# Optimization experiments

Measured on AMD Instinct MI355X. Metric: run time of the kernel, lower is better.

Reference implementation:

```python
import jax, jax.numpy as jnp
from jax import lax
import numpy as np

KSIZE = 7
SIGMA = 5.0
ALPHA = 0.05

def _gaussian_kernel(ksize, sigma):
    ax = np.arange(ksize, dtype=np.float32) - (ksize - 1) / 2.0
    g1 = np.exp(-(ax ** 2) / (2.0 * sigma ** 2))
    k2 = np.outer(g1, g1)
    k2 = k2 / k2.sum()
    return jnp.asarray(k2, dtype=jnp.float32)

def _sobel_kernel():
    sx = np.array([[-1, 0, 1], [-2, 0, 2], [-1, 0, 1]], dtype=np.float32)
    sy = np.array([[-1, -2, -1], [0, 0, 0], [1, 2, 1]], dtype=np.float32)
    return jnp.asarray(np.stack([sx, sy])[:, None], dtype=jnp.float32)  # (2,1,3,3)

def setup_inputs() -> dict:
    key = jax.random.key(0)
    x = jax.random.normal(key, (4, 1, 2048, 2048), dtype=jnp.float32)
    return {"x": x, "sobel_k": _sobel_kernel(), "gauss_k": _gaussian_kernel(KSIZE, SIGMA)}

def reference(x, sobel_k, gauss_k):
    N, _, H, W = x.shape
    dn = ('NCHW', 'OIHW', 'NCHW')
    # Image gradients: Sobel conv, 1 -> 2 channels, same padding
    g = lax.conv_general_dilated(x, sobel_k, (1, 1), [(1, 1), (1, 1)], dimension_numbers=dn)
    Ix, Iy = g[:, 0], g[:, 1]  # (N,H,W)
    # Channel products: I_xx, I_yy, I_xy
    prods = jnp.stack([Ix * Ix, Iy * Iy, Ix * Iy], axis=1)  # (N,3,H,W)
    # Second moment: depthwise 7x7 Gaussian smoothing, same padding
    p = KSIZE // 2
    gk = jnp.broadcast_to(gauss_k[None, None], (3, 1, KSIZE, KSIZE))
    S = lax.conv_general_dilated(prods, gk, (1, 1), [(p, p), (p, p)], dimension_numbers=dn, feature_group_count=3)
    Sxx, Syy, Sxy = S[:, 0], S[:, 1], S[:, 2]
    # Corner response R = det(M) - alpha * trace(M)^2
    R = Sxx * Syy - Sxy * Sxy - ALPHA * (Sxx + Syy) ** 2  # (N,H,W)
    # NMS: global lower-median threshold (torch.median semantics), 7x7 maxpool, equality mask
    n = H * W
    med = jnp.sort(R.reshape(N, -1), axis=1)[:, (n - 1) // 2]  # torch lower median
    Rt = jnp.where(R >= med[:, None, None], R, jnp.float32(0.0))
    mx = lax.reduce_window(Rt, -jnp.inf, lax.max, (1, KSIZE, KSIZE), (1, 1, 1), [(0, 0), (p, p), (p, p)])
    out = jnp.where(Rt == mx, Rt, jnp.float32(0.0))
    return out[:, None]  # (N,1,H,W)
```

## Files before the change

### kernel.cpp

```cpp
#include <hip/hip_runtime.h>

#define H 2048
#define W 2048
#define NIMG 4
#define HWPX (H*W)
#define K_RANK 2097151u

__device__ __forceinline__ unsigned fmap(float f) {
    unsigned u = __float_as_uint(f);
    return (u & 0x80000000u) ? ~u : (u | 0x80000000u);
}

__global__ void k_prep(const float* __restrict__ gk, double* __restrict__ kwd) {
    int t = threadIdx.x;
    if (t < 49) kwd[t] = (double)gk[t];
}

__global__ __launch_bounds__(512, 4) void k_harris_R(const float* __restrict__ x,
                                                     const double* __restrict__ kwd,
                                                     float* __restrict__ R,
                                                     unsigned* __restrict__ hist1)
{
    __shared__ float xs[4096];
    __align__(16) __shared__ double ixiy[2*38*72];
    unsigned* hist = (unsigned*)xs;

    const int tid = threadIdx.x;
    const int img = blockIdx.z;
    const int x0 = blockIdx.x * 64, y0 = blockIdx.y * 32;
    const float* __restrict__ X = x + (size_t)img * HWPX;

    for (int i = tid; i < 2880; i += 512) {
        int r = i / 72, c = i - r * 72;
        int gy = y0 - 4 + r, gx = x0 - 4 + c;
        float v = 0.f;
        if ((unsigned)gy < H && (unsigned)gx < W) v = X[(size_t)gy * W + gx];
        xs[i] = v;
    }
    __syncthreads();

    for (int i = tid; i < 2736; i += 512) {
        int r = i / 72, c = i - r * 72;
        double ix = 0.0, iy = 0.0;
        int gy = y0 - 3 + r, gx = x0 - 3 + c;
        if (c < 70 && (unsigned)gy < H && (unsigned)gx < W) {
            const float* p0 = &xs[r * 72 + c];
            double x00 = p0[0],   x01 = p0[1],   x02 = p0[2];
            double x10 = p0[72],                  x12 = p0[74];
            double x20 = p0[144], x21 = p0[145], x22 = p0[146];
            ix = (x02 - x00) + 2.0 * (x12 - x10) + (x22 - x20);
            iy = (x20 - x00) + 2.0 * (x21 - x01) + (x22 - x02);
        }
        ixiy[i] = ix;
        ixiy[2736 + i] = iy;
    }
    __syncthreads();

    for (int i = tid; i < 4096; i += 512) hist[i] = 0;
    __syncthreads();

    const int tc = (tid & 31) * 2;
    const int tr = (tid >> 5) * 2;

    double axx[2][2], ayy[2][2], axy[2][2];
    #pragma unroll
    for (int rr = 0; rr < 2; rr++)
        #pragma unroll
        for (int cc = 0; cc < 2; cc++) { axx[rr][cc] = 0.0; ayy[rr][cc] = 0.0; axy[rr][cc] = 0.0; }

    #pragma unroll
    for (int ii = 0; ii < 8; ii++) {
        const int prow = tr + ii;
        double vx[8], vy[8];
        const double2* rx = (const double2*)&ixiy[prow * 72 + tc];
        const double2* ry = (const double2*)&ixiy[2736 + prow * 72 + tc];
        #pragma unroll
        for (int q = 0; q < 4; q++) {
            double2 t = rx[q]; vx[2*q] = t.x; vx[2*q+1] = t.y;
            double2 u = ry[q]; vy[2*q] = u.x; vy[2*q+1] = u.y;
        }
        double xx0 = vx[0]*vx[0], yy0 = vy[0]*vy[0], xy0 = vx[0]*vy[0];
        #pragma unroll
        for (int j = 0; j < 7; j++) {
            double xx1 = vx[j+1]*vx[j+1], yy1 = vy[j+1]*vy[j+1], xy1 = vx[j+1]*vy[j+1];
            #pragma unroll
            for (int rr = 0; rr < 2; rr++) {
                const int wrow = ii - rr;
                if (wrow >= 0 && wrow <= 6) {
                    double w = kwd[wrow * 7 + j];
                    axx[rr][0] = fma(w, xx0, axx[rr][0]); axx[rr][1] = fma(w, xx1, axx[rr][1]);
                    ayy[rr][0] = fma(w, yy0, ayy[rr][0]); ayy[rr][1] = fma(w, yy1, ayy[rr][1]);
                    axy[rr][0] = fma(w, xy0, axy[rr][0]); axy[rr][1] = fma(w, xy1, axy[rr][1]);
                }
            }
            xx0 = xx1; yy0 = yy1; xy0 = xy1;
        }
    }

    float* __restrict__ Ri = R + (size_t)img * HWPX;
    #pragma unroll
    for (int rr = 0; rr < 2; rr++) {
        float2 o;
        #pragma unroll
        for (int cc = 0; cc < 2; cc++) {
            double sxx = axx[rr][cc], syy = ayy[rr][cc], sxy = axy[rr][cc];
            double t2 = sxx + syy;
            double Rv = sxx * syy - sxy * sxy - 0.05 * t2 * t2;
            ((float*)&o)[cc] = (float)Rv;
        }
        *(float2*)&Ri[(size_t)(y0 + tr + rr) * W + (x0 + tc)] = o;
        atomicAdd(&hist[fmap(o.x) >> 20], 1u);
        atomicAdd(&hist[fmap(o.y) >> 20], 1u);
    }
    __syncthreads();

    unsigned* gh = hist1 + img * 4096;
    for (int i = tid; i < 4096; i += 512) {
        unsigned v = hist[i];
        if (v) atomicAdd(&gh[i], v);
    }
}

__global__ __launch_bounds__(256) void k_scan1(const unsigned* __restrict__ hist1,
                                               int* __restrict__ metaBin,
                                               int* __restrict__ metaBase)
{
    int img = blockIdx.x, tid = threadIdx.x;
    __shared__ unsigned s[256];
    const unsigned* h = hist1 + img * 4096;
    unsigned loc[16], sum = 0;
    #pragma unroll
    for (int j = 0; j < 16; j++) { loc[j] = h[tid * 16 + j]; sum += loc[j]; }
    s[tid] = sum; __syncthreads();
    for (int off = 1; off < 256; off <<= 1) {
        unsigned v = (tid >= off) ? s[tid - off] : 0; __syncthreads();
        s[tid] += v; __syncthreads();
    }
    unsigned incl = s[tid], excl = incl - sum;
    if (K_RANK >= excl && K_RANK < incl) {
        unsigned run = excl;
        #pragma unroll
        for (int j = 0; j < 16; j++) {
            if (K_RANK < run + loc[j]) { metaBin[img] = tid * 16 + j; metaBase[img] = (int)run; break; }
            run += loc[j];
        }
    }
}

__global__ __launch_bounds__(256) void k_hist2(const float* __restrict__ R,
                                               const int* __restrict__ metaBin,
                                               unsigned* __restrict__ hist2)
{
    int img = blockIdx.x >> 10;
    unsigned b1 = (unsigned)metaBin[img];
    unsigned* h2 = hist2 + ((size_t)img << 20);
    const float4* __restrict__ R4 = (const float4*)R + (size_t)blockIdx.x * 1024;
    #pragma unroll
    for (int j = 0; j < 4; j++) {
        float4 v = R4[threadIdx.x + j * 256];
        unsigned ux = fmap(v.x), uy = fmap(v.y), uz = fmap(v.z), uw = fmap(v.w);
        if ((ux >> 20) == b1) atomicAdd(&h2[ux & 0xFFFFFu], 1u);
        if ((uy >> 20) == b1) atomicAdd(&h2[uy & 0xFFFFFu], 1u);
        if ((uz >> 20) == b1) atomicAdd(&h2[uz & 0xFFFFFu], 1u);
        if ((uw >> 20) == b1) atomicAdd(&h2[uw & 0xFFFFFu], 1u);
    }
}

__global__ __launch_bounds__(256) void k_chunks(const unsigned* __restrict__ hist2,
                                                unsigned* __restrict__ chunkSum)
{
    int img = blockIdx.y, cb = blockIdx.x, tid = threadIdx.x;
    const unsigned* h = hist2 + ((size_t)img << 20) + cb * 4096;
    unsigned s = 0;
    #pragma unroll
    for (int j = 0; j < 16; j++) s += h[tid + j * 256];
    __shared__ unsigned red[256];
    red[tid] = s; __syncthreads();
    for (int off = 128; off > 0; off >>= 1) {
        if (tid < off) red[tid] += red[tid + off];
        __syncthreads();
    }
    if (tid == 0) chunkSum[img * 256 + cb] = red[0];
}

__global__ __launch_bounds__(256) void k_scan2(const unsigned* __restrict__ hist2,
                                               const unsigned* __restrict__ chunkSum,
                                               const int* __restrict__ metaBin,
                                               const int* __restrict__ metaBase,
                                               float* __restrict__ med)
{
    int img = blockIdx.x, tid = threadIdx.x;
    __shared__ unsigned s[256];
    __shared__ int sel[2];
    unsigned target = K_RANK - (unsigned)metaBase[img];
    unsigned v = chunkSum[img * 256 + tid];
    s[tid] = v; __syncthreads();
    for (int off = 1; off < 256; off <<= 1) {
        unsigned t2 = (tid >= off) ? s[tid - off] : 0; __syncthreads();
        s[tid] += t2; __syncthreads();
    }
    unsigned incl = s[tid], excl = incl - v;
    if (target >= excl && target < incl) { sel[0] = tid; sel[1] = (int)excl; }
    __syncthreads();
    int cb = sel[0];
    unsigned cexcl = (unsigned)sel[1];

    const unsigned* h = hist2 + ((size_t)img << 20) + cb * 4096;
    unsigned loc[16], sum = 0;
    #pragma unroll
    for (int j = 0; j < 16; j++) { loc[j] = h[tid * 16 + j]; sum += loc[j]; }
    __syncthreads();
    s[tid] = sum; __syncthreads();
    for (int off = 1; off < 256; off <<= 1) {
        unsigned t2 = (tid >= off) ? s[tid - off] : 0; __syncthreads();
        s[tid] += t2; __syncthreads();
    }
    incl = s[tid] + cexcl; excl = s[tid] - sum + cexcl;
    if (target >= excl && target < incl) {
        unsigned run = excl;
        #pragma unroll
        for (int j = 0; j < 16; j++) {
            if (target < run + loc[j]) {
                unsigned c = (unsigned)cb * 4096u + (unsigned)tid * 16u + (unsigned)j;
                unsigned mu = (((unsigned)metaBin[img]) << 20) | c;
                unsigned fb = (mu & 0x80000000u) ? (mu & 0x7FFFFFFFu) : ~mu;
                med[img] = __uint_as_float(fb);
                break;
            }
            run += loc[j];
        }
    }
}

__global__ __launch_bounds__(256) void k_out(const float* __restrict__ R,
                                             const float* __restrict__ med,
                                             float* __restrict__ out)
{
    __shared__ float rt[38][39];
    __shared__ float hm[38][33];
    const int tid = threadIdx.x;
    const int img = blockIdx.z;
    const int x0 = blockIdx.x * 32, y0 = blockIdx.y * 32;
    const float m = med[img];
    const float* __restrict__ Ri = R + ((size_t)img << 22);

    for (int i = tid; i < 1444; i += 256) {
        int r = i / 38, c = i - r * 38;
        int gy = y0 - 3 + r, gx = x0 - 3 + c;
        float v = -INFINITY;
        if ((unsigned)gy < H && (unsigned)gx < W) {
            float rv = Ri[(size_t)gy * W + gx];
            v = (rv >= m) ? rv : 0.0f;
        }
        rt[r][c] = v;
    }
    __syncthreads();

    for (int i = tid; i < 1216; i += 256) {
        int r = i >> 5, c = i & 31;
        float mx = rt[r][c];
        #pragma unroll
        for (int j = 1; j < 7; j++) mx = fmaxf(mx, rt[r][c + j]);
        hm[r][c] = mx;
    }
    __syncthreads();

    const int txc = tid & 31, ty0 = tid >> 5;
    float* __restrict__ Oi = out + ((size_t)img << 22);
    #pragma unroll
    for (int q = 0; q < 4; q++) {
        int ty = ty0 + q * 8;
        float mx = hm[ty][txc];
        #pragma unroll
        for (int j = 1; j < 7; j++) mx = fmaxf(mx, hm[ty + j][txc]);
        float c = rt[ty + 3][txc + 3];
        Oi[(size_t)(y0 + ty) * W + (x0 + txc)] = (c == mx) ? c : 0.0f;
    }
}

extern "C" void kernel_launch(void* const* d_in, const int* in_sizes, int n_in,
                              void* d_out, int out_size, void* d_ws, size_t ws_size,
                              hipStream_t stream)
{
    const float* x  = (const float*)d_in[0];
    const float* gk = (const float*)d_in[2];
    float* out = (float*)d_out;

    char* ws = (char*)d_ws;
    float*    R        = (float*)ws;
    unsigned* hist1    = (unsigned*)(ws + (size_t)HWPX * NIMG * 4);
    unsigned* chunkSum = hist1 + NIMG * 4096;
    int*      metaBin  = (int*)(chunkSum + NIMG * 256);
    int*      metaBase = metaBin + NIMG;
    float*    med      = (float*)(metaBase + NIMG);
    double*   kwd      = (double*)(med + NIMG + 1);
    unsigned* hist2    = (unsigned*)d_out;

    hipMemsetAsync(hist1, 0, (size_t)NIMG * 4096 * 4, stream);
    hipMemsetAsync(hist2, 0, (size_t)NIMG * (1u << 20) * 4, stream);

    k_prep    <<<1, 64, 0, stream>>>(gk, kwd);
    k_harris_R<<<dim3(32, 64, NIMG), 512, 0, stream>>>(x, kwd, R, hist1);
    k_scan1  <<<NIMG, 256, 0, stream>>>(hist1, metaBin, metaBase);
    k_hist2  <<<4096, 256, 0, stream>>>(R, metaBin, hist2);
    k_chunks <<<dim3(256, NIMG), 256, 0, stream>>>(hist2, chunkSum);
    k_scan2  <<<NIMG, 256, 0, stream>>>(hist2, chunkSum, metaBin, metaBase, med);
    k_out    <<<dim3(64, 64, NIMG), 256, 0, stream>>>(R, med, out);
}
```

Measured before the change: 274.2 us.

## Drop Sobel staging tile, reuse LDS for histogram, fuse chunk sum with median scan

The Harris kernel now computes Sobel gradients straight from global memory, with a fast path for interior tiles, and drops the float staging buffer. The per-block histogram reuses the gradient LDS after it is consumed, which shrinks shared memory and raises the launch-bounds occupancy target from 4 to 6 blocks. The chunk-sum and second-scan kernels are merged into one launch that uses a last-block ticket, removing one kernel launch. The costs are redundant global loads for the stencil (9 per output instead of shared reuse), an extra barrier, and a single last block doing the serial median scan for all four images.

```diff
diff --git a/kernel.cpp b/kernel.cpp
--- a/kernel.cpp
+++ b/kernel.cpp
@@ -16,47 +16,54 @@
     if (t < 49) kwd[t] = (double)gk[t];
 }
 
-__global__ __launch_bounds__(512, 4) void k_harris_R(const float* __restrict__ x,
+__global__ __launch_bounds__(512, 6) void k_harris_R(const float* __restrict__ x,
                                                      const double* __restrict__ kwd,
                                                      float* __restrict__ R,
                                                      unsigned* __restrict__ hist1)
 {
-    __shared__ float xs[4096];
-    __align__(16) __shared__ double ixiy[2*38*72];
-    unsigned* hist = (unsigned*)xs;
+    __align__(16) __shared__ double ixiy[5472];
+    unsigned* hist = (unsigned*)ixiy;
 
     const int tid = threadIdx.x;
     const int img = blockIdx.z;
     const int x0 = blockIdx.x * 64, y0 = blockIdx.y * 32;
     const float* __restrict__ X = x + (size_t)img * HWPX;
 
-    for (int i = tid; i < 2880; i += 512) {
-        int r = i / 72, c = i - r * 72;
-        int gy = y0 - 4 + r, gx = x0 - 4 + c;
-        float v = 0.f;
-        if ((unsigned)gy < H && (unsigned)gx < W) v = X[(size_t)gy * W + gx];
-        xs[i] = v;
-    }
-    __syncthreads();
-
-    for (int i = tid; i < 2736; i += 512) {
-        int r = i / 72, c = i - r * 72;
-        double ix = 0.0, iy = 0.0;
-        int gy = y0 - 3 + r, gx = x0 - 3 + c;
-        if (c < 70 && (unsigned)gy < H && (unsigned)gx < W) {
-            const float* p0 = &xs[r * 72 + c];
-            double x00 = p0[0],   x01 = p0[1],   x02 = p0[2];
-            double x10 = p0[72],                  x12 = p0[74];
-            double x20 = p0[144], x21 = p0[145], x22 = p0[146];
-            ix = (x02 - x00) + 2.0 * (x12 - x10) + (x22 - x20);
-            iy = (x20 - x00) + 2.0 * (x21 - x01) + (x22 - x02);
-        }
-        ixiy[i] = ix;
-        ixiy[2736 + i] = iy;
-    }
-    __syncthreads();
-
-    for (int i = tid; i < 4096; i += 512) hist[i] = 0;
+    const bool interior = (x0 >= 4) && (x0 + 66 < W) && (y0 >= 4) && (y0 + 34 < H);
+
+    if (interior) {
+        for (int i = tid; i < 2736; i += 512) {
+            int r = i / 72, c = i - r * 72;
+            double ix = 0.0, iy = 0.0;
+            if (c < 70) {
+                const float* p = X + (size_t)(y0 - 4 + r) * W + (x0 - 4 + c);
+                double x00 = p[0],     x01 = p[1],       x02 = p[2];
+                double x10 = p[W],                        x12 = p[W + 2];
+                double x20 = p[2 * W], x21 = p[2 * W + 1], x22 = p[2 * W + 2];
+                ix = (x02 - x00) + 2.0 * (x12 - x10) + (x22 - x20);
+                iy = (x20 - x00) + 2.0 * (x21 - x01) + (x22 - x02);
+            }
+            ixiy[i] = ix;
+            ixiy[2736 + i] = iy;
+        }
+    } else {
+        for (int i = tid; i < 2736; i += 512) {
+            int r = i / 72, c = i - r * 72;
+            double ix = 0.0, iy = 0.0;
+            int gy = y0 - 3 + r, gx = x0 - 3 + c;
+            if (c < 70 && (unsigned)gy < H && (unsigned)gx < W) {
+                #define LD(yy, xx) ((((unsigned)(yy) < H) && ((unsigned)(xx) < W)) ? (double)X[(size_t)(yy) * W + (xx)] : 0.0)
+                double x00 = LD(gy - 1, gx - 1), x01 = LD(gy - 1, gx), x02 = LD(gy - 1, gx + 1);
+                double x10 = LD(gy,     gx - 1),                       x12 = LD(gy,     gx + 1);
+                double x20 = LD(gy + 1, gx - 1), x21 = LD(gy + 1, gx), x22 = LD(gy + 1, gx + 1);
+                #undef LD
+                ix = (x02 - x00) + 2.0 * (x12 - x10) + (x22 - x20);
+                iy = (x20 - x00) + 2.0 * (x21 - x01) + (x22 - x02);
+            }
+            ixiy[i] = ix;
+            ixiy[2736 + i] = iy;
+        }
+    }
     __syncthreads();
 
     const int tc = (tid & 31) * 2;
@@ -98,6 +105,7 @@
     }
 
     float* __restrict__ Ri = R + (size_t)img * HWPX;
+    unsigned bins[4];
     #pragma unroll
     for (int rr = 0; rr < 2; rr++) {
         float2 o;
@@ -109,9 +117,15 @@
             ((float*)&o)[cc] = (float)Rv;
         }
         *(float2*)&Ri[(size_t)(y0 + tr + rr) * W + (x0 + tc)] = o;
-        atomicAdd(&hist[fmap(o.x) >> 20], 1u);
-        atomicAdd(&hist[fmap(o.y) >> 20], 1u);
-    }
+        bins[rr * 2]     = fmap(o.x) >> 20;
+        bins[rr * 2 + 1] = fmap(o.y) >> 20;
+    }
+    __syncthreads();
+
+    for (int i = tid; i < 4096; i += 512) hist[i] = 0;
+    __syncthreads();
+    #pragma unroll
+    for (int q = 0; q < 4; q++) atomicAdd(&hist[bins[q]], 1u);
     __syncthreads();
 
     unsigned* gh = hist1 + img * 4096;
@@ -166,69 +180,77 @@
     }
 }
 
-__global__ __launch_bounds__(256) void k_chunks(const unsigned* __restrict__ hist2,
-                                                unsigned* __restrict__ chunkSum)
-{
-    int img = blockIdx.y, cb = blockIdx.x, tid = threadIdx.x;
+__global__ __launch_bounds__(256) void k_med(const unsigned* __restrict__ hist2,
+                                             unsigned* __restrict__ chunkSum,
+                                             const int* __restrict__ metaBin,
+                                             const int* __restrict__ metaBase,
+                                             float* __restrict__ med,
+                                             unsigned* __restrict__ ticket2)
+{
+    __shared__ unsigned s[256];
+    __shared__ unsigned lastv;
+    __shared__ int sel[2];
+    const int tid = threadIdx.x;
+    const int cb = blockIdx.x, img = blockIdx.y;
+
     const unsigned* h = hist2 + ((size_t)img << 20) + cb * 4096;
-    unsigned s = 0;
-    #pragma unroll
-    for (int j = 0; j < 16; j++) s += h[tid + j * 256];
-    __shared__ unsigned red[256];
-    red[tid] = s; __syncthreads();
+    unsigned sum = 0;
+    #pragma unroll
+    for (int j = 0; j < 16; j++) sum += h[tid + j * 256];
+    s[tid] = sum; __syncthreads();
     for (int off = 128; off > 0; off >>= 1) {
-        if (tid < off) red[tid] += red[tid + off];
-        __syncthreads();
-    }
-    if (tid == 0) chunkSum[img * 256 + cb] = red[0];
-}
-
-__global__ __launch_bounds__(256) void k_scan2(const unsigned* __restrict__ hist2,
-                                               const unsigned* __restrict__ chunkSum,
-                                               const int* __restrict__ metaBin,
-                                               const int* __restrict__ metaBase,
-                                               float* __restrict__ med)
-{
-    int img = blockIdx.x, tid = threadIdx.x;
-    __shared__ unsigned s[256];
-    __shared__ int sel[2];
-    unsigned target = K_RANK - (unsigned)metaBase[img];
-    unsigned v = chunkSum[img * 256 + tid];
-    s[tid] = v; __syncthreads();
-    for (int off = 1; off < 256; off <<= 1) {
-        unsigned t2 = (tid >= off) ? s[tid - off] : 0; __syncthreads();
-        s[tid] += t2; __syncthreads();
-    }
-    unsigned incl = s[tid], excl = incl - v;
-    if (target >= excl && target < incl) { sel[0] = tid; sel[1] = (int)excl; }
-    __syncthreads();
-    int cb = sel[0];
-    unsigned cexcl = (unsigned)sel[1];
-
-    const unsigned* h = hist2 + ((size_t)img << 20) + cb * 4096;
-    unsigned loc[16], sum = 0;
-    #pragma unroll
-    for (int j = 0; j < 16; j++) { loc[j] = h[tid * 16 + j]; sum += loc[j]; }
-    __syncthreads();
-    s[tid] = sum; __syncthreads();
-    for (int off = 1; off < 256; off <<= 1) {
-        unsigned t2 = (tid >= off) ? s[tid - off] : 0; __syncthreads();
-        s[tid] += t2; __syncthreads();
-    }
-    incl = s[tid] + cexcl; excl = s[tid] - sum + cexcl;
-    if (target >= excl && target < incl) {
-        unsigned run = excl;
-        #pragma unroll
-        for (int j = 0; j < 16; j++) {
-            if (target < run + loc[j]) {
-                unsigned c = (unsigned)cb * 4096u + (unsigned)tid * 16u + (unsigned)j;
-                unsigned mu = (((unsigned)metaBin[img]) << 20) | c;
-                unsigned fb = (mu & 0x80000000u) ? (mu & 0x7FFFFFFFu) : ~mu;
-                med[img] = __uint_as_float(fb);
-                break;
+        if (tid < off) s[tid] += s[tid + off];
+        __syncthreads();
+    }
+    if (tid == 0) {
+        atomicExch(&chunkSum[img * 256 + cb], s[0]);
+        __threadfence();
+        lastv = atomicAdd(ticket2, 1u);
+    }
+    __syncthreads();
+    if (lastv != NIMG * 256 - 1) return;
+
+    for (int im = 0; im < NIMG; im++) {
+        unsigned target = K_RANK - (unsigned)metaBase[im];
+        unsigned v = atomicAdd(&chunkSum[im * 256 + tid], 0u);
+        __syncthreads();
+        s[tid] = v; __syncthreads();
+        for (int off = 1; off < 256; off <<= 1) {
+            unsigned t2 = (tid >= off) ? s[tid - off] : 0; __syncthreads();
+            s[tid] += t2; __syncthreads();
+        }
+        unsigned incl = s[tid], excl = incl - v;
+        if (target >= excl && target < incl) { sel[0] = tid; sel[1] = (int)excl; }
+        __syncthreads();
+        int scb = sel[0];
+        unsigned cexcl = (unsigned)sel[1];
+
+        const unsigned* hh = hist2 + ((size_t)im << 20) + scb * 4096;
+        unsigned loc[16], lsum = 0;
+        #pragma unroll
+        for (int j = 0; j < 16; j++) { loc[j] = hh[tid * 16 + j]; lsum += loc[j]; }
+        __syncthreads();
+        s[tid] = lsum; __syncthreads();
+        for (int off = 1; off < 256; off <<= 1) {
+            unsigned t2 = (tid >= off) ? s[tid - off] : 0; __syncthreads();
+            s[tid] += t2; __syncthreads();
+        }
+        incl = s[tid] + cexcl; excl = s[tid] - lsum + cexcl;
+        if (target >= excl && target < incl) {
+            unsigned run = excl;
+            #pragma unroll
+            for (int j = 0; j < 16; j++) {
+                if (target < run + loc[j]) {
+                    unsigned c = (unsigned)scb * 4096u + (unsigned)tid * 16u + (unsigned)j;
+                    unsigned mu = (((unsigned)metaBin[im]) << 20) | c;
+                    unsigned fb = (mu & 0x80000000u) ? (mu & 0x7FFFFFFFu) : ~mu;
+                    med[im] = __uint_as_float(fb);
+                    break;
+                }
+                run += loc[j];
             }
-            run += loc[j];
-        }
+        }
+        __syncthreads();
     }
 }
 
@@ -289,21 +311,22 @@
     char* ws = (char*)d_ws;
     float*    R        = (float*)ws;
     unsigned* hist1    = (unsigned*)(ws + (size_t)HWPX * NIMG * 4);
-    unsigned* chunkSum = hist1 + NIMG * 4096;
-    int*      metaBin  = (int*)(chunkSum + NIMG * 256);
+    unsigned* ticket1  = hist1 + NIMG * 4096;
+    unsigned* ticket2  = ticket1 + 4;
+    unsigned* chunkSum = ticket2 + 1;
+    int*      metaBin  = (int*)(chunkSum + 1024);
     int*      metaBase = metaBin + NIMG;
     float*    med      = (float*)(metaBase + NIMG);
-    double*   kwd      = (double*)(med + NIMG + 1);
+    double*   kwd      = (double*)(ws + (size_t)HWPX * NIMG * 4 + 71680);
     unsigned* hist2    = (unsigned*)d_out;
 
-    hipMemsetAsync(hist1, 0, (size_t)NIMG * 4096 * 4, stream);
+    hipMemsetAsync(hist1, 0, (size_t)NIMG * 4096 * 4 + 32, stream);
     hipMemsetAsync(hist2, 0, (size_t)NIMG * (1u << 20) * 4, stream);
 
     k_prep    <<<1, 64, 0, stream>>>(gk, kwd);
     k_harris_R<<<dim3(32, 64, NIMG), 512, 0, stream>>>(x, kwd, R, hist1);
-    k_scan1  <<<NIMG, 256, 0, stream>>>(hist1, metaBin, metaBase);
-    k_hist2  <<<4096, 256, 0, stream>>>(R, metaBin, hist2);
-    k_chunks <<<dim3(256, NIMG), 256, 0, stream>>>(hist2, chunkSum);
-    k_scan2  <<<NIMG, 256, 0, stream>>>(hist2, chunkSum, metaBin, metaBase, med);
-    k_out    <<<dim3(64, 64, NIMG), 256, 0, stream>>>(R, med, out);
-}
+    k_scan1   <<<NIMG, 256, 0, stream>>>(hist1, metaBin, metaBase);
+    k_hist2   <<<4096, 256, 0, stream>>>(R, metaBin, hist2);
+    k_med     <<<dim3(256, NIMG), 256, 0, stream>>>(hist2, chunkSum, metaBin, metaBase, med, ticket2);
+    k_out     <<<dim3(64, 64, NIMG), 256, 0, stream>>>(R, med, out);
+}
```

Measured after the change: 487.4 us. +77.8%, slower.
